# Kernel tuning notes

Measured on AMD Instinct MI355X. Metric: run time of the kernel, lower is better.

The kernel has to match this reference:

```python
import jax, jax.numpy as jnp
import numpy as np

B, S, DIM = 2, 2048, 2048
INTER = 1024          # moe_inter_dim
E = 8                 # n_routed_experts
K = 2                 # n_activated_experts
N_SHARED = 1
ROUTE_SCALE = 1.0


def setup_inputs() -> dict:
    key = jax.random.key(0)
    ks = jax.random.split(key, 8)
    s_in = 1.0 / np.sqrt(DIM)
    s_hid = 1.0 / np.sqrt(INTER)
    return {
        "x": jax.random.normal(ks[0], (B, S, DIM), dtype=jnp.float32),
        "gate_w": jax.random.normal(ks[1], (E, DIM), dtype=jnp.float32) * s_in,
        "w1": jax.random.normal(ks[2], (E, INTER, DIM), dtype=jnp.float32) * s_in,
        "w2": jax.random.normal(ks[3], (E, DIM, INTER), dtype=jnp.float32) * s_hid,
        "w3": jax.random.normal(ks[4], (E, INTER, DIM), dtype=jnp.float32) * s_in,
        "ws1": jax.random.normal(ks[5], (N_SHARED * INTER, DIM), dtype=jnp.float32) * s_in,
        "ws2": jax.random.normal(ks[6], (DIM, N_SHARED * INTER), dtype=jnp.float32) * s_hid,
        "ws3": jax.random.normal(ks[7], (N_SHARED * INTER, DIM), dtype=jnp.float32) * s_in,
    }


def reference(x, gate_w, w1, w2, w3, ws1, ws2, ws3):
    shape = x.shape
    xf = x.reshape(-1, DIM)                         # [T, d]
    # --- Gate: softmax scores, top-k (single group => plain top-k) ---
    scores = jax.nn.softmax(xf @ gate_w.T, axis=-1)  # [T, E]
    weights, idx = jax.lax.top_k(scores, K)          # [T, K]
    weights = weights * ROUTE_SCALE
    # --- Routed experts (dense compute + one-hot combine) ---
    h = jnp.einsum('td,eid->eti', xf, w1)            # [E, T, inter]
    g = jax.nn.silu(h) * jnp.einsum('td,eid->eti', xf, w3)
    eo = jnp.einsum('eti,edi->etd', g, w2)           # [E, T, d]
    comb = jnp.einsum('tke,tk->te', jax.nn.one_hot(idx, E, dtype=xf.dtype), weights)
    y = jnp.einsum('etd,te->td', eo, comb)           # [T, d]
    # --- Shared expert MLP (SwiGLU) ---
    z = (jax.nn.silu(xf @ ws1.T) * (xf @ ws3.T)) @ ws2.T
    return (y + z).reshape(shape)
```

## Files before the change

kernel.cpp:

```cpp
#include <hip/hip_runtime.h>
#include <stdint.h>

#define T_TOK 4096
#define DIM   2048
#define INTER 1024
#define NE    9
#define NPAIR 12288

typedef float v4f __attribute__((ext_vector_type(4)));
typedef short v8s __attribute__((ext_vector_type(8)));

__device__ __forceinline__ unsigned short f2bf(float f) {
    unsigned u = __float_as_uint(f);
    u += 0x7fffu + ((u >> 16) & 1u);
    return (unsigned short)(u >> 16);
}

__device__ __forceinline__ void gload_lds16(const void* g, void* l) {
    __builtin_amdgcn_global_load_lds(
        (const __attribute__((address_space(1))) void*)g,
        (__attribute__((address_space(3))) void*)l, 16, 0, 0);
}

__global__ __launch_bounds__(256) void prep_kernel(
        const float* __restrict__ w1,  const float* __restrict__ ws1, unsigned short* __restrict__ w1b,
        const float* __restrict__ w3,  const float* __restrict__ ws3, unsigned short* __restrict__ w3b,
        const float* __restrict__ x,   const float* __restrict__ gw,
        float* __restrict__ wt,        int* __restrict__ ei,
        unsigned short* __restrict__ xb,
        int* __restrict__ meta) {
    if (blockIdx.y < 2) {
        if (blockIdx.x == 0 && blockIdx.y == 0 && threadIdx.x < 18) meta[threadIdx.x] = 0;
        int which = blockIdx.y;
        const float* wmain = (which == 0) ? w1  : w3;
        const float* wsh   = (which == 0) ? ws1 : ws3;
        unsigned short* dst = (which == 0) ? w1b : w3b;
        long long i = (long long)blockIdx.x * 256 + threadIdx.x;
        long long base = i * 4;
        int e = (int)(base >> 21);
        long long within = base & ((1ll << 21) - 1);
        const float* src = (e < 8) ? (wmain + ((long long)e << 21) + within) : (wsh + within);
        float4 f = *(const float4*)src;
        ushort4 u;
        u.x = f2bf(f.x); u.y = f2bf(f.y); u.z = f2bf(f.z); u.w = f2bf(f.w);
        *(ushort4*)(dst + base) = u;
        return;
    }
    int t = blockIdx.x;
    if (t >= T_TOK) return;
    __shared__ float xs[DIM];
    __shared__ float lg[8];
    const float* xrow = x + (size_t)t * DIM;
    for (int i = threadIdx.x; i < DIM / 4; i += 256)
        ((float4*)xs)[i] = ((const float4*)xrow)[i];
    __syncthreads();
    for (int i = threadIdx.x; i < DIM / 4; i += 256) {
        float4 f = ((const float4*)xs)[i];
        ushort4 u;
        u.x = f2bf(f.x); u.y = f2bf(f.y); u.z = f2bf(f.z); u.w = f2bf(f.w);
        ((ushort4*)(xb + (size_t)t * DIM))[i] = u;
    }
    int e = threadIdx.x >> 5;
    int l = threadIdx.x & 31;
    const float* g = gw + (size_t)e * DIM;
    float p = 0.f;
    #pragma unroll 8
    for (int d = l; d < DIM; d += 32) p += xs[d] * g[d];
    for (int m = 16; m >= 1; m >>= 1) p += __shfl_xor(p, m, 32);
    if (l == 0) lg[e] = p;
    __syncthreads();
    if (threadIdx.x == 0) {
        float mx = lg[0];
        for (int i = 1; i < 8; i++) mx = fmaxf(mx, lg[i]);
        float pr[8], s = 0.f;
        for (int i = 0; i < 8; i++) { pr[i] = __expf(lg[i] - mx); s += pr[i]; }
        float inv = 1.f / s;
        float b1 = -1.f, b2 = -1.f; int i1 = 0, i2 = 0;
        for (int i = 0; i < 8; i++) {
            float v = pr[i] * inv;
            if (v > b1)      { b2 = b1; i2 = i1; b1 = v; i1 = i; }
            else if (v > b2) { b2 = v;  i2 = i; }
        }
        wt[t * 3 + 0] = b1; wt[t * 3 + 1] = b2; wt[t * 3 + 2] = 1.f;
        ei[t * 3 + 0] = i1; ei[t * 3 + 1] = i2; ei[t * 3 + 2] = 8;
    }
}

__global__ __launch_bounds__(256) void count_kernel(const int* __restrict__ ei,
                                                    int* __restrict__ meta) {
    __shared__ int lcnt[NE];
    if (threadIdx.x < NE) lcnt[threadIdx.x] = 0;
    __syncthreads();
    int t = blockIdx.x * 256 + threadIdx.x;
    #pragma unroll
    for (int s = 0; s < 3; s++) atomicAdd(&lcnt[ei[t * 3 + s]], 1);
    __syncthreads();
    if (threadIdx.x < NE) atomicAdd(&meta[threadIdx.x], lcnt[threadIdx.x]);
}

__global__ __launch_bounds__(256) void fill_kernel(const int* __restrict__ ei,
                                                   const float* __restrict__ wt,
                                                   int* __restrict__ meta,
                                                   int* __restrict__ pair_tok,
                                                   float* __restrict__ pair_w,
                                                   int* __restrict__ slots) {
    __shared__ int lcnt[NE], lbase[NE], loffs[NE];
    if (threadIdx.x < NE) lcnt[threadIdx.x] = 0;
    __syncthreads();
    int t = blockIdx.x * 256 + threadIdx.x;
    int es[3], lp[3];
    #pragma unroll
    for (int s = 0; s < 3; s++) {
        es[s] = ei[t * 3 + s];
        lp[s] = atomicAdd(&lcnt[es[s]], 1);
    }
    __syncthreads();
    if (threadIdx.x < NE)
        lbase[threadIdx.x] = atomicAdd(&meta[9 + threadIdx.x], lcnt[threadIdx.x]);
    if (threadIdx.x == 0) {
        int a = 0;
        #pragma unroll
        for (int e = 0; e < NE; e++) { loffs[e] = a; a += meta[e]; }
    }
    __syncthreads();
    #pragma unroll
    for (int s = 0; s < 3; s++) {
        int g = loffs[es[s]] + lbase[es[s]] + lp[s];
        pair_tok[g] = t;
        pair_w[g] = wt[t * 3 + s];
        slots[t * 3 + s] = g;
    }
}

__global__ __launch_bounds__(256, 3) void gemm1_kernel(
        const unsigned short* __restrict__ xb,
        const unsigned short* __restrict__ w1b,
        const unsigned short* __restrict__ w3b,
        unsigned short* __restrict__ G,
        const int* __restrict__ meta,
        const int* __restrict__ pair_tok,
        const float* __restrict__ pair_w,
        const float* __restrict__ w2f,
        const float* __restrict__ ws2,
        unsigned short* __restrict__ w2b) {
    int e  = blockIdx.z;
    int by = blockIdx.y;
    int bx = blockIdx.x;

    if (by >= 32) {
        int flat = (e * 8 + (by - 32)) * 16 + bx;
        long long vbase = (long long)flat * 4096 + threadIdx.x;
        #pragma unroll
        for (int it = 0; it < 16; ++it) {
            long long i = vbase + it * 256;
            long long base = i * 4;
            int ew = (int)(base >> 21);
            long long within = base & ((1ll << 21) - 1);
            const float* src = (ew < 8) ? (w2f + ((long long)ew << 21) + within) : (ws2 + within);
            float4 f = *(const float4*)src;
            ushort4 u;
            u.x = f2bf(f.x); u.y = f2bf(f.y); u.z = f2bf(f.z); u.w = f2bf(f.w);
            *(ushort4*)(w2b + base) = u;
        }
        return;
    }
    int cnt = meta[e];
    int m0 = by * 128;
    if (m0 >= cnt) return;
    int off = 0;
    for (int i = 0; i < e; i++) off += meta[i];
    int n0 = bx * 64;

    __shared__ __align__(16) unsigned short As[128 * 64];
    __shared__ __align__(16) unsigned short B1s[64 * 64];
    __shared__ __align__(16) unsigned short B3s[64 * 64];

    int tid = threadIdx.x;
    int wave = tid >> 6, lane = tid & 63;
    int kc = (lane & 7) ^ (lane >> 3);

    const unsigned short* sbase;
    unsigned short* ldst;
    unsigned soff[8];
    if (wave < 2) {
        sbase = xb;
        ldst = As + wave * 4096;
        #pragma unroll
        for (int j = 0; j < 8; j++) {
            int row = (wave * 8 + j) * 8 + (lane >> 3);
            int p = m0 + row; p = p < cnt ? p : cnt - 1;
            int tok = pair_tok[off + p];
            soff[j] = (unsigned)tok * DIM + (unsigned)(kc * 8);
        }
    } else {
        const unsigned short* wsrc = (wave == 2) ? w1b : w3b;
        ldst = (wave == 2) ? B1s : B3s;
        sbase = wsrc + ((size_t)e * INTER + n0 + (lane >> 3)) * DIM + kc * 8;
    }

    int wm = wave >> 1, wn = wave & 1;
    int mb = wm * 64, nb = wn * 32;
    v4f zero4 = {0.f, 0.f, 0.f, 0.f};
    v4f acc1[4][2], acc3[4][2];
    #pragma unroll
    for (int i = 0; i < 4; i++)
        #pragma unroll
        for (int j = 0; j < 2; j++) { acc1[i][j] = zero4; acc3[i][j] = zero4; }

    for (int k0 = 0; k0 < DIM; k0 += 64) {
        if (wave < 2) {
            #pragma unroll
            for (int j = 0; j < 8; j++)
                gload_lds16(sbase + soff[j] + k0, ldst + j * 512);
        } else {
            #pragma unroll
            for (int j = 0; j < 8; j++)
                gload_lds16(sbase + (unsigned)(j * 8 * DIM) + k0, ldst + j * 512);
        }
        __syncthreads();
        #pragma unroll
        for (int s = 0; s < 2; s++) {
            int kk = s * 4 + (lane >> 4);
            v8s a[4], b1[2], b3[2];
            #pragma unroll
            for (int mt = 0; mt < 4; mt++) {
                int r = mb + mt * 16 + (lane & 15);
                a[mt] = *(const v8s*)&As[r * 64 + ((kk ^ (r & 7)) << 3)];
            }
            #pragma unroll
            for (int nt = 0; nt < 2; nt++) {
                int n = nb + nt * 16 + (lane & 15);
                int o = n * 64 + ((kk ^ (n & 7)) << 3);
                b1[nt] = *(const v8s*)&B1s[o];
                b3[nt] = *(const v8s*)&B3s[o];
            }
            #pragma unroll
            for (int mt = 0; mt < 4; mt++)
                #pragma unroll
                for (int nt = 0; nt < 2; nt++) {
                    acc1[mt][nt] = __builtin_amdgcn_mfma_f32_16x16x32_bf16(a[mt], b1[nt], acc1[mt][nt], 0, 0, 0);
                    acc3[mt][nt] = __builtin_amdgcn_mfma_f32_16x16x32_bf16(a[mt], b3[nt], acc3[mt][nt], 0, 0, 0);
                }
        }
        __syncthreads();
    }

    #pragma unroll
    for (int mt = 0; mt < 4; mt++) {
        #pragma unroll
        for (int r = 0; r < 4; r++) {
            int row = mb + mt * 16 + ((lane >> 4) << 2) + r;
            int p = m0 + row;
            if (p < cnt) {
                float w = pair_w[off + p];
                size_t gbase = (size_t)(off + p) * INTER + n0 + nb;
                #pragma unroll
                for (int nt = 0; nt < 2; nt++) {
                    float h1 = acc1[mt][nt][r];
                    float h3 = acc3[mt][nt][r];
                    float gv = h1 / (1.f + __expf(-h1)) * h3 * w;
                    G[gbase + nt * 16 + (lane & 15)] = f2bf(gv);
                }
            }
        }
    }
}

__global__ __launch_bounds__(256, 3) void gemm2_kernel(
        const unsigned short* __restrict__ G,
        const unsigned short* __restrict__ w2b,
        unsigned short* __restrict__ eo,
        const int* __restrict__ meta) {
    int e  = blockIdx.z;
    int by = blockIdx.y;
    int bx = blockIdx.x;

    int cnt = meta[e];
    int m0 = by * 128;
    if (m0 >= cnt) return;
    int off = 0;
    for (int i = 0; i < e; i++) off += meta[i];
    int n0 = bx * 128;

    __shared__ __align__(16) unsigned short As[128 * 64];
    __shared__ __align__(16) unsigned short Bs[128 * 64];

    int tid = threadIdx.x;
    int wave = tid >> 6, lane = tid & 63;
    int kc = (lane & 7) ^ (lane >> 3);

    const unsigned short* sbase;
    unsigned short* ldst;
    unsigned soff[8];
    if (wave < 2) {
        sbase = G;
        ldst = As + wave * 4096;
        #pragma unroll
        for (int j = 0; j < 8; j++) {
            int row = (wave * 8 + j) * 8 + (lane >> 3);
            int p = m0 + row; p = p < cnt ? p : cnt - 1;
            soff[j] = (unsigned)(off + p) * INTER + (unsigned)(kc * 8);
        }
    } else {
        int g0 = (wave - 2) * 64;
        ldst = Bs + (wave - 2) * 4096;
        sbase = w2b + ((size_t)e * DIM + n0 + g0 + (lane >> 3)) * INTER + kc * 8;
    }

    int wm = wave >> 1, wn = wave & 1;
    int mb = wm * 64, nbw = wn * 64;
    v4f zero4 = {0.f, 0.f, 0.f, 0.f};
    v4f acc[4][4];
    #pragma unroll
    for (int i = 0; i < 4; i++)
        #pragma unroll
        for (int j = 0; j < 4; j++) acc[i][j] = zero4;

    for (int k0 = 0; k0 < INTER; k0 += 64) {
        if (wave < 2) {
            #pragma unroll
            for (int j = 0; j < 8; j++)
                gload_lds16(sbase + soff[j] + k0, ldst + j * 512);
        } else {
            #pragma unroll
            for (int j = 0; j < 8; j++)
                gload_lds16(sbase + (unsigned)(j * 8 * INTER) + k0, ldst + j * 512);
        }
        __syncthreads();
        #pragma unroll
        for (int s = 0; s < 2; s++) {
            int kk = s * 4 + (lane >> 4);
            v8s a[4], b[4];
            #pragma unroll
            for (int mt = 0; mt < 4; mt++) {
                int r = mb + mt * 16 + (lane & 15);
                a[mt] = *(const v8s*)&As[r * 64 + ((kk ^ (r & 7)) << 3)];
            }
            #pragma unroll
            for (int nt = 0; nt < 4; nt++) {
                int n = nbw + nt * 16 + (lane & 15);
                b[nt] = *(const v8s*)&Bs[n * 64 + ((kk ^ (n & 7)) << 3)];
            }
            #pragma unroll
            for (int mt = 0; mt < 4; mt++)
                #pragma unroll
                for (int nt = 0; nt < 4; nt++)
                    acc[mt][nt] = __builtin_amdgcn_mfma_f32_16x16x32_bf16(a[mt], b[nt], acc[mt][nt], 0, 0, 0);
        }
        __syncthreads();
    }

    #pragma unroll
    for (int mt = 0; mt < 4; mt++) {
        #pragma unroll
        for (int r = 0; r < 4; r++) {
            int row = mb + mt * 16 + ((lane >> 4) << 2) + r;
            int p = m0 + row;
            if (p < cnt) {
                unsigned short* obase = eo + (size_t)(off + p) * DIM + n0 + nbw;
                #pragma unroll
                for (int nt = 0; nt < 4; nt++)
                    obase[nt * 16 + (lane & 15)] = f2bf(acc[mt][nt][r]);
            }
        }
    }
}

__global__ __launch_bounds__(256) void combine_kernel(const unsigned short* __restrict__ eo,
                                                      const int* __restrict__ slots,
                                                      float* __restrict__ out) {
    int t = blockIdx.x;
    int p0 = slots[t * 3 + 0], p1 = slots[t * 3 + 1], p2 = slots[t * 3 + 2];
    const ushort4* r0 = (const ushort4*)(eo + (size_t)p0 * DIM);
    const ushort4* r1 = (const ushort4*)(eo + (size_t)p1 * DIM);
    const ushort4* r2 = (const ushort4*)(eo + (size_t)p2 * DIM);
    float4* o = (float4*)(out + (size_t)t * DIM);
    for (int i = threadIdx.x; i < DIM / 4; i += 256) {
        ushort4 a = r0[i], b = r1[i], c = r2[i];
        float4 v;
        v.x = __uint_as_float((unsigned)a.x << 16) + __uint_as_float((unsigned)b.x << 16) + __uint_as_float((unsigned)c.x << 16);
        v.y = __uint_as_float((unsigned)a.y << 16) + __uint_as_float((unsigned)b.y << 16) + __uint_as_float((unsigned)c.y << 16);
        v.z = __uint_as_float((unsigned)a.z << 16) + __uint_as_float((unsigned)b.z << 16) + __uint_as_float((unsigned)c.z << 16);
        v.w = __uint_as_float((unsigned)a.w << 16) + __uint_as_float((unsigned)b.w << 16) + __uint_as_float((unsigned)c.w << 16);
        o[i] = v;
    }
}

extern "C" void kernel_launch(void* const* d_in, const int* in_sizes, int n_in,
                              void* d_out, int out_size, void* d_ws, size_t ws_size,
                              hipStream_t stream) {
    const float* x   = (const float*)d_in[0];
    const float* gw  = (const float*)d_in[1];
    const float* w1  = (const float*)d_in[2];
    const float* w2  = (const float*)d_in[3];
    const float* w3  = (const float*)d_in[4];
    const float* ws1 = (const float*)d_in[5];
    const float* ws2 = (const float*)d_in[6];
    const float* ws3 = (const float*)d_in[7];
    float* out = (float*)d_out;

    char* p = (char*)d_ws;
    auto alloc = [&](size_t bytes) {
        void* r = (void*)p;
        p += (bytes + 255) & ~(size_t)255;
        return r;
    };
    unsigned short* xb  = (unsigned short*)alloc((size_t)T_TOK * DIM * 2);
    unsigned short* w1b = (unsigned short*)alloc((size_t)NE * INTER * DIM * 2);
    unsigned short* w3b = (unsigned short*)alloc((size_t)NE * INTER * DIM * 2);
    unsigned short* w2b = (unsigned short*)alloc((size_t)NE * DIM * INTER * 2);
    unsigned short* G   = (unsigned short*)alloc((size_t)NPAIR * INTER * 2);
    int*   ei    = (int*)alloc((size_t)T_TOK * 3 * 4);
    float* wt    = (float*)alloc((size_t)T_TOK * 3 * 4);
    int*   ptok  = (int*)alloc((size_t)NPAIR * 4);
    float* pw    = (float*)alloc((size_t)NPAIR * 4);
    int*   slots = (int*)alloc((size_t)NPAIR * 4);
    int*   meta  = (int*)alloc(32 * 4);
    unsigned short* eo = w1b;

    int wgrid = (NE * INTER * DIM / 4) / 256;
    prep_kernel<<<dim3(wgrid, 3), 256, 0, stream>>>(w1, ws1, w1b, w3, ws3, w3b,
                                                    x, gw, wt, ei, xb, meta);
    count_kernel<<<T_TOK / 256, 256, 0, stream>>>(ei, meta);
    fill_kernel<<<T_TOK / 256, 256, 0, stream>>>(ei, wt, meta, ptok, pw, slots);
    gemm1_kernel<<<dim3(INTER / 64, 40, NE), 256, 0, stream>>>(xb, w1b, w3b, G, meta, ptok, pw,
                                                               w2, ws2, w2b);
    gemm2_kernel<<<dim3(DIM / 128, 32, NE), 256, 0, stream>>>(G, w2b, eo, meta);
    combine_kernel<<<T_TOK, 256, 0, stream>>>(eo, slots, out);
}
```

Measured before the change: 440.1 us.

## Rewrite expert down-projection GEMM with 256x256 tiles and double-buffered LDS pipeline

Rewrites the second grouped GEMM to use 512-thread blocks computing 256x256 output tiles. It double-buffers A and B tiles in LDS and interleaves the global-to-LDS loads for future k-chunks with MFMA batches, using explicit barriers, waitcnt and setprio. The aim is to hide global load latency and raise data reuse per block. The cost is 128KB of LDS per block, which limits occupancy, and more waste on partially filled expert tiles. A-row indices are no longer clamped to the expert count, so the last tile may read past the valid rows.

```diff
diff --git a/kernel.cpp b/kernel.cpp
--- a/kernel.cpp
+++ b/kernel.cpp
@@ -266,104 +266,166 @@
     }
 }
 
-__global__ __launch_bounds__(256, 3) void gemm2_kernel(
+__global__ __launch_bounds__(512, 2) void gemm2_kernel(
         const unsigned short* __restrict__ G,
         const unsigned short* __restrict__ w2b,
         unsigned short* __restrict__ eo,
         const int* __restrict__ meta) {
-    int e  = blockIdx.z;
-    int by = blockIdx.y;
-    int bx = blockIdx.x;
-
+    int e = blockIdx.z;
     int cnt = meta[e];
-    int m0 = by * 128;
+    int m0 = blockIdx.y * 256;
     if (m0 >= cnt) return;
     int off = 0;
     for (int i = 0; i < e; i++) off += meta[i];
-    int n0 = bx * 128;
-
-    __shared__ __align__(16) unsigned short As[128 * 64];
-    __shared__ __align__(16) unsigned short Bs[128 * 64];
+    int n0 = blockIdx.x * 256;
+
+    __shared__ __align__(16) unsigned short As[2][256 * 64];
+    __shared__ __align__(16) unsigned short Bs[2][256 * 64];
 
     int tid = threadIdx.x;
     int wave = tid >> 6, lane = tid & 63;
-    int kc = (lane & 7) ^ (lane >> 3);
-
-    const unsigned short* sbase;
-    unsigned short* ldst;
-    unsigned soff[8];
-    if (wave < 2) {
-        sbase = G;
-        ldst = As + wave * 4096;
-        #pragma unroll
-        for (int j = 0; j < 8; j++) {
-            int row = (wave * 8 + j) * 8 + (lane >> 3);
-            int p = m0 + row; p = p < cnt ? p : cnt - 1;
-            soff[j] = (unsigned)(off + p) * INTER + (unsigned)(kc * 8);
-        }
-    } else {
-        int g0 = (wave - 2) * 64;
-        ldst = Bs + (wave - 2) * 4096;
-        sbase = w2b + ((size_t)e * DIM + n0 + g0 + (lane >> 3)) * INTER + kc * 8;
-    }
-
-    int wm = wave >> 1, wn = wave & 1;
-    int mb = wm * 64, nbw = wn * 64;
+    int wm = wave >> 2, wn = wave & 3;
+    int l15 = lane & 15;
+    int kS0 = (lane >> 4);
+    int kS1 = 4 + (lane >> 4);
+
+    int c0 = tid, c1 = tid + 512;
+    int r0 = c0 >> 3, r1 = c1 >> 3;
+    unsigned kc0 = (unsigned)(((c0 & 7) ^ (r0 & 7)) * 8);
+    unsigned kc1 = (unsigned)(((c1 & 7) ^ (r1 & 7)) * 8);
+    const unsigned short* Agb = G + (size_t)(off + m0) * INTER;
+    const unsigned short* Bgb = w2b + ((size_t)e * DIM + n0) * INTER;
+
+#define G2_STAGE_A(buf, half, k0) do { \
+    gload_lds16(Agb + (size_t)((half) * 128 + r0) * INTER + (k0) + kc0, &As[buf][(half) * 8192 + c0 * 8]); \
+    gload_lds16(Agb + (size_t)((half) * 128 + r1) * INTER + (k0) + kc1, &As[buf][(half) * 8192 + c1 * 8]); \
+} while (0)
+#define G2_STAGE_B(buf, half, k0) do { \
+    gload_lds16(Bgb + (size_t)((half) * 128 + r0) * INTER + (k0) + kc0, &Bs[buf][(half) * 8192 + c0 * 8]); \
+    gload_lds16(Bgb + (size_t)((half) * 128 + r1) * INTER + (k0) + kc1, &Bs[buf][(half) * 8192 + c1 * 8]); \
+} while (0)
+#define G2_SBAR()  asm volatile("s_barrier" ::: "memory")
+#define G2_LGKM0() do { asm volatile("s_waitcnt lgkmcnt(0)" ::: "memory"); \
+                        __builtin_amdgcn_sched_barrier(0); } while (0)
+#define G2_VMC4()  asm volatile("s_waitcnt vmcnt(4)" ::: "memory")
+#define G2_LDF(tile, row, kch) (*(const v8s*)&(tile)[(row) * 64 + (((kch) ^ ((row) & 7)) << 3)])
+#define G2_MFMA16(av, b_lo, b_hi, nlo, nhi) do { \
+    __builtin_amdgcn_s_setprio(1); \
+    _Pragma("unroll") \
+    for (int mf = 0; mf < 8; mf++) { \
+        acc[mf][nlo] = __builtin_amdgcn_mfma_f32_16x16x32_bf16(av[mf], b_lo, acc[mf][nlo], 0, 0, 0); \
+        acc[mf][nhi] = __builtin_amdgcn_mfma_f32_16x16x32_bf16(av[mf], b_hi, acc[mf][nhi], 0, 0, 0); \
+    } \
+    __builtin_amdgcn_s_setprio(0); \
+} while (0)
+
+    v4f acc[8][4];
     v4f zero4 = {0.f, 0.f, 0.f, 0.f};
-    v4f acc[4][4];
-    #pragma unroll
-    for (int i = 0; i < 4; i++)
+    #pragma unroll
+    for (int i = 0; i < 8; i++)
         #pragma unroll
         for (int j = 0; j < 4; j++) acc[i][j] = zero4;
 
-    for (int k0 = 0; k0 < INTER; k0 += 64) {
-        if (wave < 2) {
-            #pragma unroll
-            for (int j = 0; j < 8; j++)
-                gload_lds16(sbase + soff[j] + k0, ldst + j * 512);
-        } else {
-            #pragma unroll
-            for (int j = 0; j < 8; j++)
-                gload_lds16(sbase + (unsigned)(j * 8 * INTER) + k0, ldst + j * 512);
-        }
-        __syncthreads();
-        #pragma unroll
-        for (int s = 0; s < 2; s++) {
-            int kk = s * 4 + (lane >> 4);
-            v8s a[4], b[4];
-            #pragma unroll
-            for (int mt = 0; mt < 4; mt++) {
-                int r = mb + mt * 16 + (lane & 15);
-                a[mt] = *(const v8s*)&As[r * 64 + ((kk ^ (r & 7)) << 3)];
-            }
-            #pragma unroll
-            for (int nt = 0; nt < 4; nt++) {
-                int n = nbw + nt * 16 + (lane & 15);
-                b[nt] = *(const v8s*)&Bs[n * 64 + ((kk ^ (n & 7)) << 3)];
-            }
-            #pragma unroll
-            for (int mt = 0; mt < 4; mt++)
-                #pragma unroll
-                for (int nt = 0; nt < 4; nt++)
-                    acc[mt][nt] = __builtin_amdgcn_mfma_f32_16x16x32_bf16(a[mt], b[nt], acc[mt][nt], 0, 0, 0);
-        }
-        __syncthreads();
-    }
-
-    #pragma unroll
-    for (int mt = 0; mt < 4; mt++) {
+    G2_STAGE_A(0, 0, 0); G2_STAGE_A(0, 1, 0); G2_STAGE_B(0, 0, 0); G2_STAGE_B(0, 1, 0);
+    G2_STAGE_A(1, 0, 64); G2_STAGE_A(1, 1, 64);
+    G2_VMC4();
+    G2_SBAR();
+
+    for (int it = 0; it < 8; ++it) {
+        int k1 = (2 * it + 1) * 64;
+        int k2 = (2 * it + 2) * 64;
+        int k3 = (2 * it + 3) * 64;
+        bool more = (it < 7);
+        v8s a0[8], a1[8], bl, bh;
+
+        #pragma unroll
+        for (int mf = 0; mf < 8; mf++) a0[mf] = G2_LDF(As[0], wm * 128 + mf * 16 + l15, kS0);
+        bl = G2_LDF(Bs[0], wn * 64 + 0 * 16 + l15, kS0);
+        bh = G2_LDF(Bs[0], wn * 64 + 1 * 16 + l15, kS0);
+        G2_STAGE_B(1, 0, k1);
+        G2_SBAR(); G2_LGKM0();
+        G2_MFMA16(a0, bl, bh, 0, 1);
+        G2_SBAR();
+
+        #pragma unroll
+        for (int mf = 0; mf < 8; mf++) a1[mf] = G2_LDF(As[0], wm * 128 + mf * 16 + l15, kS1);
+        bl = G2_LDF(Bs[0], wn * 64 + 2 * 16 + l15, kS0);
+        bh = G2_LDF(Bs[0], wn * 64 + 3 * 16 + l15, kS0);
+        G2_STAGE_B(1, 1, k1);
+        G2_SBAR(); G2_LGKM0();
+        G2_MFMA16(a0, bl, bh, 2, 3);
+        G2_SBAR();
+
+        bl = G2_LDF(Bs[0], wn * 64 + 0 * 16 + l15, kS1);
+        bh = G2_LDF(Bs[0], wn * 64 + 1 * 16 + l15, kS1);
+        if (more) G2_STAGE_A(0, 0, k2);
+        G2_SBAR(); G2_LGKM0();
+        G2_MFMA16(a1, bl, bh, 0, 1);
+        G2_SBAR();
+
+        bl = G2_LDF(Bs[0], wn * 64 + 2 * 16 + l15, kS1);
+        bh = G2_LDF(Bs[0], wn * 64 + 3 * 16 + l15, kS1);
+        if (more) G2_STAGE_A(0, 1, k2);
+        G2_SBAR(); G2_LGKM0();
+        G2_MFMA16(a1, bl, bh, 2, 3);
+        G2_VMC4();
+        G2_SBAR();
+
+        #pragma unroll
+        for (int mf = 0; mf < 8; mf++) a0[mf] = G2_LDF(As[1], wm * 128 + mf * 16 + l15, kS0);
+        bl = G2_LDF(Bs[1], wn * 64 + 0 * 16 + l15, kS0);
+        bh = G2_LDF(Bs[1], wn * 64 + 1 * 16 + l15, kS0);
+        if (more) G2_STAGE_B(0, 0, k2);
+        G2_SBAR(); G2_LGKM0();
+        G2_MFMA16(a0, bl, bh, 0, 1);
+        G2_SBAR();
+
+        #pragma unroll
+        for (int mf = 0; mf < 8; mf++) a1[mf] = G2_LDF(As[1], wm * 128 + mf * 16 + l15, kS1);
+        bl = G2_LDF(Bs[1], wn * 64 + 2 * 16 + l15, kS0);
+        bh = G2_LDF(Bs[1], wn * 64 + 3 * 16 + l15, kS0);
+        if (more) G2_STAGE_B(0, 1, k2);
+        G2_SBAR(); G2_LGKM0();
+        G2_MFMA16(a0, bl, bh, 2, 3);
+        G2_SBAR();
+
+        bl = G2_LDF(Bs[1], wn * 64 + 0 * 16 + l15, kS1);
+        bh = G2_LDF(Bs[1], wn * 64 + 1 * 16 + l15, kS1);
+        if (more) G2_STAGE_A(1, 0, k3);
+        G2_SBAR(); G2_LGKM0();
+        G2_MFMA16(a1, bl, bh, 0, 1);
+        G2_SBAR();
+
+        bl = G2_LDF(Bs[1], wn * 64 + 2 * 16 + l15, kS1);
+        bh = G2_LDF(Bs[1], wn * 64 + 3 * 16 + l15, kS1);
+        if (more) G2_STAGE_A(1, 1, k3);
+        G2_SBAR(); G2_LGKM0();
+        G2_MFMA16(a1, bl, bh, 2, 3);
+        G2_VMC4();
+        G2_SBAR();
+    }
+
+    #pragma unroll
+    for (int mf = 0; mf < 8; mf++) {
         #pragma unroll
         for (int r = 0; r < 4; r++) {
-            int row = mb + mt * 16 + ((lane >> 4) << 2) + r;
+            int row = wm * 128 + mf * 16 + ((lane >> 4) << 2) + r;
             int p = m0 + row;
             if (p < cnt) {
-                unsigned short* obase = eo + (size_t)(off + p) * DIM + n0 + nbw;
+                unsigned short* ob = eo + (size_t)(off + p) * DIM + n0 + wn * 64;
                 #pragma unroll
-                for (int nt = 0; nt < 4; nt++)
-                    obase[nt * 16 + (lane & 15)] = f2bf(acc[mt][nt][r]);
+                for (int nf = 0; nf < 4; nf++)
+                    ob[nf * 16 + l15] = f2bf(acc[mf][nf][r]);
             }
         }
     }
+#undef G2_STAGE_A
+#undef G2_STAGE_B
+#undef G2_SBAR
+#undef G2_LGKM0
+#undef G2_VMC4
+#undef G2_LDF
+#undef G2_MFMA16
 }
 
 __global__ __launch_bounds__(256) void combine_kernel(const unsigned short* __restrict__ eo,
@@ -425,6 +487,6 @@
     fill_kernel<<<T_TOK / 256, 256, 0, stream>>>(ei, wt, meta, ptok, pw, slots);
     gemm1_kernel<<<dim3(INTER / 64, 40, NE), 256, 0, stream>>>(xb, w1b, w3b, G, meta, ptok, pw,
                                                                w2, ws2, w2b);
-    gemm2_kernel<<<dim3(DIM / 128, 32, NE), 256, 0, stream>>>(G, w2b, eo, meta);
+    gemm2_kernel<<<dim3(DIM / 256, 16, NE), 512, 0, stream>>>(G, w2b, eo, meta);
     combine_kernel<<<T_TOK, 256, 0, stream>>>(eo, slots, out);
 }
```

After: 450.8 us. 2.4% more time.
